# Performance work log

Measured on AMD Instinct MI355X. Metric: run time of the kernel, lower is better.

Reference implementation:

```python
import jax, jax.numpy as jnp
import numpy as np

EMBED_DIM = 1024
CONTEXT_DIM = 768
NUM_HEADS = 16
HEAD_DIM = EMBED_DIM // NUM_HEADS
B, N, M = 8, 4096, 77


def setup_inputs() -> dict:
    key = jax.random.key(0)
    ks = jax.random.split(key, 12)
    s_in = 1.0 / np.sqrt(EMBED_DIM)
    s_ctx = 1.0 / np.sqrt(CONTEXT_DIM)
    x = jax.random.normal(ks[0], (B, N, EMBED_DIM), dtype=jnp.float32)
    context = jax.random.normal(ks[1], (B, M, CONTEXT_DIM), dtype=jnp.float32)
    # realistic padding mask: each example has a random valid prefix length in [1, M]
    lengths = jax.random.randint(ks[2], (B,), 1, M + 1)
    context_mask = jnp.arange(M)[None, :] < lengths[:, None]  # (B, M) bool
    Wq = jax.random.uniform(ks[3], (EMBED_DIM, EMBED_DIM), jnp.float32, -s_in, s_in)
    bq = jax.random.uniform(ks[4], (EMBED_DIM,), jnp.float32, -s_in, s_in)
    Wk = jax.random.uniform(ks[5], (CONTEXT_DIM, EMBED_DIM), jnp.float32, -s_ctx, s_ctx)
    bk = jax.random.uniform(ks[6], (EMBED_DIM,), jnp.float32, -s_ctx, s_ctx)
    Wv = jax.random.uniform(ks[7], (CONTEXT_DIM, EMBED_DIM), jnp.float32, -s_ctx, s_ctx)
    bv = jax.random.uniform(ks[8], (EMBED_DIM,), jnp.float32, -s_ctx, s_ctx)
    Wo = jax.random.uniform(ks[9], (EMBED_DIM, EMBED_DIM), jnp.float32, -s_in, s_in)
    bo = jax.random.uniform(ks[10], (EMBED_DIM,), jnp.float32, -s_in, s_in)
    return {"x": x, "context": context, "context_mask": context_mask,
            "Wq": Wq, "bq": bq, "Wk": Wk, "bk": bk, "Wv": Wv, "bv": bv,
            "Wo": Wo, "bo": bo}


def reference(x, context, context_mask, Wq, bq, Wk, bk, Wv, bv, Wo, bo):
    H, d = NUM_HEADS, HEAD_DIM
    scale = d ** -0.5
    Bx, Nx, _ = x.shape
    Mx = context.shape[1]
    # projections
    q = (x @ Wq + bq).reshape(Bx, Nx, H, d).transpose(0, 2, 1, 3)        # (B,H,N,d)
    k = (context @ Wk + bk).reshape(Bx, Mx, H, d).transpose(0, 2, 1, 3)  # (B,H,M,d)
    v = (context @ Wv + bv).reshape(Bx, Mx, H, d).transpose(0, 2, 1, 3)  # (B,H,M,d)
    # scores with padding mask
    attn = jnp.einsum('bhnd,bhmd->bhnm', q, k) * scale                   # (B,H,N,M)
    attn = jnp.where(context_mask[:, None, None, :], attn, -jnp.inf)
    attn = jax.nn.softmax(attn, axis=-1)
    out = jnp.einsum('bhnm,bhmd->bhnd', attn, v)                          # (B,H,N,d)
    out = out.transpose(0, 2, 1, 3).reshape(Bx, Nx, H * d)                # (B,N,E)
    return out @ Wo + bo
```

## Files before the change

### kernel.cpp

```cpp
#include <hip/hip_runtime.h>

typedef __bf16 bf16x8 __attribute__((ext_vector_type(8)));
typedef float f32x4 __attribute__((ext_vector_type(4)));

#define EMB 1024
#define CTXD 768
#define NH 16
#define HD 64
#define BB 8
#define NN 4096
#define MM 77
#define MPAD 96

static __device__ __forceinline__ unsigned short f2bf(float f) {
    unsigned u = __builtin_bit_cast(unsigned, f);
    u += 0x7FFFu + ((u >> 16) & 1u);
    return (unsigned short)(u >> 16);
}

__global__ void mask_lengths_kernel(const unsigned char* __restrict__ mask,
                                    int* __restrict__ lengths) {
    int ln = threadIdx.x & 63;
    int anyOdd = 0, anyF = 0;
    for (int i = ln; i < BB * MM; i += 64) {
        unsigned char v = mask[i];
        if (v == 0x80u || v == 0x3Fu) anyF = 1;
        if ((i & 3) && v) anyOdd = 1;
    }
    anyF = __any(anyF); anyOdd = __any(anyOdd);
    int layout = anyF ? 2 : (anyOdd ? 1 : 0);
    int b = ln >> 3, j = ln & 7, cnt = 0;
    for (int m = j; m < MM; m += 8) {
        int idx = b * MM + m;
        int valid;
        if (layout == 1)      valid = mask[idx] != 0;
        else if (layout == 0) valid = ((const int*)mask)[idx] != 0;
        else                  valid = ((const float*)mask)[idx] != 0.0f;
        cnt += valid ? 1 : 0;
    }
    cnt += __shfl_xor(cnt, 1, 64);
    cnt += __shfl_xor(cnt, 2, 64);
    cnt += __shfl_xor(cnt, 4, 64);
    if (j == 0) lengths[b] = cnt;
}

__global__ void cast_f32_to_bf16(const float* __restrict__ in,
                                 unsigned short* __restrict__ out, int n8) {
    for (int i = blockIdx.x * blockDim.x + threadIdx.x; i < n8;
         i += gridDim.x * blockDim.x) {
        float4 v0 = ((const float4*)in)[2 * i];
        float4 v1 = ((const float4*)in)[2 * i + 1];
        union { unsigned short u[8]; int4 v; } r;
        r.u[0] = f2bf(v0.x); r.u[1] = f2bf(v0.y);
        r.u[2] = f2bf(v0.z); r.u[3] = f2bf(v0.w);
        r.u[4] = f2bf(v1.x); r.u[5] = f2bf(v1.y);
        r.u[6] = f2bf(v1.z); r.u[7] = f2bf(v1.w);
        ((int4*)out)[i] = r.v;
    }
}

__global__ void cast_ctx_kernel(const float* __restrict__ in,
                                unsigned short* __restrict__ out) {
    int i = blockIdx.x * 256 + threadIdx.x;
    if (i >= 640 * CTXD / 8) return;
    int row = (i * 8) / CTXD;
    union { unsigned short u[8]; int4 v; } r;
    if (row < BB * MM) {
        float4 v0 = ((const float4*)in)[2 * i];
        float4 v1 = ((const float4*)in)[2 * i + 1];
        r.u[0] = f2bf(v0.x); r.u[1] = f2bf(v0.y);
        r.u[2] = f2bf(v0.z); r.u[3] = f2bf(v0.w);
        r.u[4] = f2bf(v1.x); r.u[5] = f2bf(v1.y);
        r.u[6] = f2bf(v1.z); r.u[7] = f2bf(v1.w);
    } else {
        r.v = make_int4(0, 0, 0, 0);
    }
    ((int4*)out)[i] = r.v;
}

struct TPtrs { const float* src[4]; unsigned short* dst[4]; };
__global__ void transpose4_kernel(TPtrs tp) {
    __shared__ float t[32][33];
    int z = blockIdx.z;
    int R = (z < 2) ? 1024 : 768, C = 1024;
    int r0 = blockIdx.y * 32;
    if (r0 >= R) return;
    const float* W = tp.src[z];
    unsigned short* Wt = tp.dst[z];
    int tx = threadIdx.x, ty = threadIdx.y;
    int c0 = blockIdx.x * 32;
#pragma unroll
    for (int i = 0; i < 32; i += 8)
        t[ty + i][tx] = W[(size_t)(r0 + ty + i) * C + c0 + tx];
    __syncthreads();
#pragma unroll
    for (int i = 0; i < 32; i += 8)
        Wt[(size_t)(c0 + ty + i) * R + r0 + tx] = f2bf(t[tx][ty + i]);
}

template <int MODE>
__global__ __launch_bounds__(512, 2) void gemm256_kernel(
    const unsigned short* __restrict__ A, const unsigned short* __restrict__ Bt,
    const float* __restrict__ bias, void* __restrict__ Cout,
    int M, int N, int K) {
    __shared__ unsigned short lds[4][2][256 * 32];
    const int tid = threadIdx.x, wv = tid >> 6, ln = tid & 63;
    const int numN = N >> 8;
    int bid = blockIdx.x;
    const int nwg = (M >> 8) * numN;
    if ((nwg & 7) == 0) { int cpx = nwg >> 3; bid = (bid & 7) * cpx + (bid >> 3); }
    const int nt_ = bid % numN, mt = bid / numN;
    const int m0 = mt << 8, n0 = nt_ << 8;
    const int wr = wv >> 2, wc = wv & 3;
    const int NT = K >> 5;

    const int srow = wv * 16 + (ln >> 2);
    const int sslot = ln & 3;

    auto stageA = [&](int t) {
#pragma unroll
        for (int half = 0; half < 2; ++half) {
            int row = half * 128 + srow;
            int gc = sslot ^ ((row >> 1) & 3);
            __builtin_amdgcn_global_load_lds(
                (const __attribute__((address_space(1))) void*)(
                    A + (size_t)(m0 + row) * K + (t << 5) + gc * 8),
                (__attribute__((address_space(3))) void*)(
                    &lds[t & 3][0][(half * 128 + wv * 16) * 32]),
                16, 0, 0);
        }
    };
    auto stageB = [&](int t) {
#pragma unroll
        for (int half = 0; half < 2; ++half) {
            int row = half * 128 + srow;
            int gc = sslot ^ ((row >> 1) & 3);
            __builtin_amdgcn_global_load_lds(
                (const __attribute__((address_space(1))) void*)(
                    Bt + (size_t)(n0 + row) * K + (t << 5) + gc * 8),
                (__attribute__((address_space(3))) void*)(
                    &lds[t & 3][1][(half * 128 + wv * 16) * 32]),
                16, 0, 0);
        }
    };
    auto readA = [&](const unsigned short* As, int i) -> bf16x8 {
        int arow = wr * 128 + i * 16 + (ln & 15);
        int aslot = (ln >> 4) ^ ((arow >> 1) & 3);
        return *(const bf16x8*)(As + arow * 32 + aslot * 8);
    };
    auto readB = [&](const unsigned short* Bs, int j) -> bf16x8 {
        int brow = wc * 64 + j * 16 + (ln & 15);
        int bslot = (ln >> 4) ^ ((brow >> 1) & 3);
        return *(const bf16x8*)(Bs + brow * 32 + bslot * 8);
    };

    f32x4 acc[8][4] = {};
    bf16x8 afA[4], afB[4], bfrC[4], afN[4], bfrN[4];

    stageA(0); stageB(0); stageA(1); stageB(1); stageA(2); stageB(2);
    asm volatile("s_waitcnt vmcnt(4)" ::: "memory");
    __builtin_amdgcn_sched_barrier(0);
    __builtin_amdgcn_s_barrier();
#pragma unroll
    for (int i = 0; i < 4; ++i) afA[i] = readA(lds[0][0], i);
#pragma unroll
    for (int j = 0; j < 4; ++j) bfrC[j] = readB(lds[0][1], j);

#pragma unroll 4
    for (int t = 0; t < NT; ++t) {
        const unsigned short* As = lds[t & 3][0];
        const unsigned short* Asn = lds[(t + 1) & 3][0];
        const unsigned short* Bsn = lds[(t + 1) & 3][1];
        if (t + 3 < NT) stageA(t + 3);
#pragma unroll
        for (int i = 0; i < 4; ++i) afB[i] = readA(As, i + 4);
        __builtin_amdgcn_s_barrier();
        __builtin_amdgcn_s_setprio(1);
#pragma unroll
        for (int i = 0; i < 4; ++i)
#pragma unroll
            for (int j = 0; j < 4; ++j)
                acc[i][j] = __builtin_amdgcn_mfma_f32_16x16x32_bf16(
                    afA[i], bfrC[j], acc[i][j], 0, 0, 0);
        __builtin_amdgcn_s_setprio(0);
        __builtin_amdgcn_s_barrier();
        if (t + 3 < NT) stageB(t + 3);
        if (t + 1 < NT) {
#pragma unroll
            for (int i = 0; i < 4; ++i) afN[i] = readA(Asn, i);
#pragma unroll
            for (int j = 0; j < 4; ++j) bfrN[j] = readB(Bsn, j);
        }
        if (t + 3 < NT) { asm volatile("s_waitcnt vmcnt(4)" ::: "memory"); }
        else            { asm volatile("s_waitcnt vmcnt(0)" ::: "memory"); }
        __builtin_amdgcn_sched_barrier(0);
        __builtin_amdgcn_s_barrier();
        __builtin_amdgcn_s_setprio(1);
#pragma unroll
        for (int i = 0; i < 4; ++i)
#pragma unroll
            for (int j = 0; j < 4; ++j)
                acc[i + 4][j] = __builtin_amdgcn_mfma_f32_16x16x32_bf16(
                    afB[i], bfrC[j], acc[i + 4][j], 0, 0, 0);
        __builtin_amdgcn_s_setprio(0);
        __builtin_amdgcn_s_barrier();
#pragma unroll
        for (int i = 0; i < 4; ++i) afA[i] = afN[i];
#pragma unroll
        for (int j = 0; j < 4; ++j) bfrC[j] = bfrN[j];
    }

    float bvals[4];
#pragma unroll
    for (int j = 0; j < 4; ++j)
        bvals[j] = bias[n0 + wc * 64 + j * 16 + (ln & 15)];
#pragma unroll
    for (int i = 0; i < 8; ++i)
#pragma unroll
        for (int j = 0; j < 4; ++j)
#pragma unroll
            for (int r = 0; r < 4; ++r) {
                int row = m0 + wr * 128 + i * 16 + (ln >> 4) * 4 + r;
                int col = n0 + wc * 64 + j * 16 + (ln & 15);
                float v = acc[i][j][r] + bvals[j];
                if constexpr (MODE == 0)
                    ((unsigned short*)Cout)[(size_t)row * N + col] = f2bf(v);
                else
                    ((float*)Cout)[(size_t)row * N + col] = v;
            }
}

static __device__ __forceinline__ void stage_tile(
    const unsigned short* __restrict__ G, int ldg, unsigned short* lds,
    int r0, int kt, int wv, int ln) {
    int rown = ln >> 2;
    int koff = (ln & 3) * 8;
#pragma unroll
    for (int r = 0; r < 2; ++r) {
        int cw = wv * 2 + r;
        const unsigned short* src =
            G + (size_t)(r0 + cw * 16 + rown) * ldg + kt + koff;
        __builtin_amdgcn_global_load_lds(
            (const __attribute__((address_space(1))) void*)src,
            (__attribute__((address_space(3))) void*)(lds + cw * 512),
            16, 0, 0);
    }
}

template <int MODE>
__global__ __launch_bounds__(256) void gemm_bt_kernel(
    const unsigned short* __restrict__ A, const unsigned short* __restrict__ Bt,
    const float* __restrict__ bias, void* __restrict__ Cout,
    int M, int N, int K) {
    __shared__ unsigned short As[128 * 32];
    __shared__ unsigned short Bs[128 * 32];
    const int tid = threadIdx.x, wv = tid >> 6, ln = tid & 63;
    const int numM = M >> 7, numN = N >> 7;
    int bid = blockIdx.x;
    const int nwg = numM * numN;
    if ((nwg & 7) == 0) { int cpx = nwg >> 3; bid = (bid & 7) * cpx + (bid >> 3); }
    const int nt = bid % numN, mt = bid / numN;
    const int m0 = mt << 7, n0 = nt << 7;
    const int wr = wv >> 1, wc = wv & 1;

    f32x4 acc[4][4] = {};
    for (int kt = 0; kt < K; kt += 32) {
        __syncthreads();
        stage_tile(A, K, As, m0, kt, wv, ln);
        stage_tile(Bt, K, Bs, n0, kt, wv, ln);
        __syncthreads();
        bf16x8 af[4], bfr[4];
#pragma unroll
        for (int i = 0; i < 4; ++i)
            af[i] = *(const bf16x8*)(As + (wr * 64 + i * 16 + (ln & 15)) * 32 +
                                     (ln >> 4) * 8);
#pragma unroll
        for (int j = 0; j < 4; ++j)
            bfr[j] = *(const bf16x8*)(Bs + (wc * 64 + j * 16 + (ln & 15)) * 32 +
                                      (ln >> 4) * 8);
#pragma unroll
        for (int i = 0; i < 4; ++i)
#pragma unroll
            for (int j = 0; j < 4; ++j)
                acc[i][j] = __builtin_amdgcn_mfma_f32_16x16x32_bf16(
                    af[i], bfr[j], acc[i][j], 0, 0, 0);
    }

    float bvals[4];
#pragma unroll
    for (int j = 0; j < 4; ++j)
        bvals[j] = bias[n0 + wc * 64 + j * 16 + (ln & 15)];

#pragma unroll
    for (int i = 0; i < 4; ++i) {
#pragma unroll
        for (int j = 0; j < 4; ++j) {
#pragma unroll
            for (int r = 0; r < 4; ++r) {
                int row = m0 + wr * 64 + i * 16 + (ln >> 4) * 4 + r;
                int col = n0 + wc * 64 + j * 16 + (ln & 15);
                float v = acc[i][j][r] + bvals[j];
                if (row < BB * MM) {
                    int bb = row / MM, m = row - bb * MM;
                    int hh = col >> 6, d = col & 63;
                    if constexpr (MODE == 2)
                        ((unsigned short*)Cout)[((size_t)(bb * NH + hh) * MPAD + m) * HD + d] = f2bf(v);
                    else
                        ((unsigned short*)Cout)[((size_t)(bb * NH + hh) * HD + d) * MPAD + m] = f2bf(v);
                }
            }
        }
    }
}

__global__ __launch_bounds__(256, 3) void attn_kernel(
    const unsigned short* __restrict__ Q, const unsigned short* __restrict__ Kw,
    const unsigned short* __restrict__ Vt, const int* __restrict__ lengths,
    unsigned short* __restrict__ Out) {
    const int bh = blockIdx.y;
    const int b = bh >> 4, h = bh & 15;
    const int q0 = blockIdx.x * 128;
    const int tid = threadIdx.x, wv = tid >> 6, ln = tid & 63;
    const int len = lengths[b];
    const int kscnt = (len + 31) >> 5;

    __shared__ unsigned short Ps[128][104];

    const unsigned short* Ksrc = Kw + (size_t)bh * (MPAD * HD);
    const unsigned short* Vsrc = Vt + (size_t)bh * (HD * MPAD);

    bf16x8 aq[2][2];
#pragma unroll
    for (int qi = 0; qi < 2; ++qi) {
        const int qr = q0 + wv * 32 + qi * 16 + (ln & 15);
        const unsigned short* qptr =
            Q + (size_t)(b * NN + qr) * EMB + h * HD + (ln >> 4) * 8;
        aq[qi][0] = *(const bf16x8*)(qptr);
        aq[qi][1] = *(const bf16x8*)(qptr + 32);
    }

    bf16x8 vf[3][4];
#pragma unroll
    for (int j = 0; j < 4; ++j)
        vf[0][j] = *(const bf16x8*)(Vsrc + (j * 16 + (ln & 15)) * MPAD +
                                    (ln >> 4) * 8);
    if (kscnt > 1) {
#pragma unroll
        for (int j = 0; j < 4; ++j)
            vf[1][j] = *(const bf16x8*)(Vsrc + (j * 16 + (ln & 15)) * MPAD + 32 +
                                        (ln >> 4) * 8);
    }
    if (kscnt > 2) {
#pragma unroll
        for (int j = 0; j < 4; ++j)
            vf[2][j] = *(const bf16x8*)(Vsrc + (j * 16 + (ln & 15)) * MPAD + 64 +
                                        (ln >> 4) * 8);
    }

    f32x4 s[2][5] = {};
#pragma unroll
    for (int t = 0; t < 5; ++t) {
        if (t * 16 < len) {
            const unsigned short* kp =
                Ksrc + (t * 16 + (ln & 15)) * HD + (ln >> 4) * 8;
            bf16x8 k0 = *(const bf16x8*)(kp);
            bf16x8 k1 = *(const bf16x8*)(kp + 32);
#pragma unroll
            for (int qi = 0; qi < 2; ++qi) {
                s[qi][t] = __builtin_amdgcn_mfma_f32_16x16x32_bf16(
                    aq[qi][0], k0, s[qi][t], 0, 0, 0);
                s[qi][t] = __builtin_amdgcn_mfma_f32_16x16x32_bf16(
                    aq[qi][1], k1, s[qi][t], 0, 0, 0);
            }
        }
    }

    const float scale = 0.125f;
    float mx[2][4], sum[2][4];
#pragma unroll
    for (int qi = 0; qi < 2; ++qi)
#pragma unroll
        for (int r = 0; r < 4; ++r) { mx[qi][r] = -1e30f; sum[qi][r] = 0.f; }
#pragma unroll
    for (int t = 0; t < 5; ++t) {
        int m = t * 16 + (ln & 15);
        bool valid = m < len;
#pragma unroll
        for (int qi = 0; qi < 2; ++qi)
#pragma unroll
            for (int r = 0; r < 4; ++r) {
                float v = valid ? s[qi][t][r] * scale : -1e30f;
                s[qi][t][r] = v;
                mx[qi][r] = fmaxf(mx[qi][r], v);
            }
    }
#pragma unroll
    for (int d = 1; d < 16; d <<= 1)
#pragma unroll
        for (int qi = 0; qi < 2; ++qi)
#pragma unroll
            for (int r = 0; r < 4; ++r)
                mx[qi][r] = fmaxf(mx[qi][r], __shfl_xor(mx[qi][r], d, 64));
#pragma unroll
    for (int t = 0; t < 5; ++t)
#pragma unroll
        for (int qi = 0; qi < 2; ++qi)
#pragma unroll
            for (int r = 0; r < 4; ++r) {
                float p = __expf(s[qi][t][r] - mx[qi][r]);
                s[qi][t][r] = p;
                sum[qi][r] += p;
            }
#pragma unroll
    for (int d = 1; d < 16; d <<= 1)
#pragma unroll
        for (int qi = 0; qi < 2; ++qi)
#pragma unroll
            for (int r = 0; r < 4; ++r)
                sum[qi][r] += __shfl_xor(sum[qi][r], d, 64);

    float rinv[2][4];
#pragma unroll
    for (int qi = 0; qi < 2; ++qi)
#pragma unroll
        for (int r = 0; r < 4; ++r) rinv[qi][r] = 1.0f / sum[qi][r];

#pragma unroll
    for (int t = 0; t < 6; ++t)
#pragma unroll
        for (int qi = 0; qi < 2; ++qi)
#pragma unroll
            for (int r = 0; r < 4; ++r) {
                int row = wv * 32 + qi * 16 + (ln >> 4) * 4 + r;
                float v = (t < 5) ? s[qi][t][r] * rinv[qi][r] : 0.0f;
                Ps[row][t * 16 + (ln & 15)] = f2bf(v);
            }

    f32x4 o[2][4] = {};
    for (int ks = 0; ks < kscnt; ++ks) {
#pragma unroll
        for (int qi = 0; qi < 2; ++qi) {
            bf16x8 pf = *(const bf16x8*)(&Ps[wv * 32 + qi * 16 + (ln & 15)]
                                            [ks * 32 + (ln >> 4) * 8]);
#pragma unroll
            for (int j = 0; j < 4; ++j)
                o[qi][j] = __builtin_amdgcn_mfma_f32_16x16x32_bf16(
                    vf[ks][j], pf, o[qi][j], 0, 0, 0);
        }
    }

#pragma unroll
    for (int qi = 0; qi < 2; ++qi) {
        const int qrow = q0 + wv * 32 + qi * 16 + (ln & 15);
        unsigned short* obase =
            Out + (size_t)(b * NN + qrow) * EMB + h * HD + (ln >> 4) * 4;
#pragma unroll
        for (int j = 0; j < 4; ++j) {
            union { unsigned short u[4]; unsigned long long ll; } pk;
#pragma unroll
            for (int r = 0; r < 4; ++r) pk.u[r] = f2bf(o[qi][j][r]);
            *(unsigned long long*)(obase + j * 16) = pk.ll;
        }
    }
}

extern "C" void kernel_launch(void* const* d_in, const int* in_sizes, int n_in,
                              void* d_out, int out_size, void* d_ws, size_t ws_size,
                              hipStream_t stream) {
    const float* x    = (const float*)d_in[0];
    const float* ctx  = (const float*)d_in[1];
    const unsigned char* cmask = (const unsigned char*)d_in[2];
    const float* Wq = (const float*)d_in[3];
    const float* bq = (const float*)d_in[4];
    const float* Wk = (const float*)d_in[5];
    const float* bk = (const float*)d_in[6];
    const float* Wv = (const float*)d_in[7];
    const float* bv = (const float*)d_in[8];
    const float* Wo = (const float*)d_in[9];
    const float* bo = (const float*)d_in[10];

    char* ws = (char*)d_ws;
    unsigned short* Xbf   = (unsigned short*)(ws);
    unsigned short* Wq_t  = (unsigned short*)(ws + 67108864);
    unsigned short* Wo_t  = (unsigned short*)(ws + 69206016);
    unsigned short* Wk_t  = (unsigned short*)(ws + 71303168);
    unsigned short* Wv_t  = (unsigned short*)(ws + 72876032);
    unsigned short* Cbf   = (unsigned short*)(ws + 74448896);
    unsigned short* Kw    = (unsigned short*)(ws + 75431936);
    unsigned short* Vtw   = (unsigned short*)(ws + 77004800);
    int* lengths          = (int*)(ws + 78577664);
    unsigned short* Qb    = (unsigned short*)d_out;

    mask_lengths_kernel<<<1, 64, 0, stream>>>(cmask, lengths);
    cast_f32_to_bf16<<<2048, 256, 0, stream>>>(x, Xbf, (BB * NN * EMB) / 8);
    cast_ctx_kernel<<<240, 256, 0, stream>>>(ctx, Cbf);
    TPtrs tp;
    tp.src[0] = Wq; tp.src[1] = Wo; tp.src[2] = Wk; tp.src[3] = Wv;
    tp.dst[0] = Wq_t; tp.dst[1] = Wo_t; tp.dst[2] = Wk_t; tp.dst[3] = Wv_t;
    transpose4_kernel<<<dim3(32, 32, 4), dim3(32, 8), 0, stream>>>(tp);
    hipMemsetAsync(Kw, 0, 2 * 1572864, stream);

    gemm256_kernel<0><<<512, 512, 0, stream>>>(Xbf, Wq_t, bq, Qb, 32768, 1024, 1024);
    gemm_bt_kernel<2><<<40, 256, 0, stream>>>(Cbf, Wk_t, bk, Kw, 640, 1024, 768);
    gemm_bt_kernel<3><<<40, 256, 0, stream>>>(Cbf, Wv_t, bv, Vtw, 640, 1024, 768);

    attn_kernel<<<dim3(32, 128), 256, 0, stream>>>(Qb, Kw, Vtw, lengths, Xbf);

    gemm256_kernel<1><<<512, 512, 0, stream>>>(Xbf, Wo_t, bo, d_out, 32768, 1024, 1024);
}
```

Measured before the change: 326.5 us.

## Fuse x f32-to-bf16 cast into Q GEMM, merge K/V GEMMs, simplify pipeline

Removes the standalone cast kernel for x. A new Q-projection GEMM loads f32 A tiles into registers, converts them to bf16 and writes them to LDS, which avoids a full write and re-read of the 64MB bf16 copy. The K and V projection GEMMs are merged into a single launch, and the existing 256-tile GEMM's register double-buffered fragment prefetch is replaced by simpler in-iteration LDS reads with adjusted waitcnts. The trade-off is that the Q GEMM now reads twice the A bytes and does conversion work inside its main loop, and the output GEMM loses its fragment prefetch overlap.

```diff
diff --git a/kernel.cpp b/kernel.cpp
--- a/kernel.cpp
+++ b/kernel.cpp
@@ -42,21 +42,6 @@
     cnt += __shfl_xor(cnt, 2, 64);
     cnt += __shfl_xor(cnt, 4, 64);
     if (j == 0) lengths[b] = cnt;
-}
-
-__global__ void cast_f32_to_bf16(const float* __restrict__ in,
-                                 unsigned short* __restrict__ out, int n8) {
-    for (int i = blockIdx.x * blockDim.x + threadIdx.x; i < n8;
-         i += gridDim.x * blockDim.x) {
-        float4 v0 = ((const float4*)in)[2 * i];
-        float4 v1 = ((const float4*)in)[2 * i + 1];
-        union { unsigned short u[8]; int4 v; } r;
-        r.u[0] = f2bf(v0.x); r.u[1] = f2bf(v0.y);
-        r.u[2] = f2bf(v0.z); r.u[3] = f2bf(v0.w);
-        r.u[4] = f2bf(v1.x); r.u[5] = f2bf(v1.y);
-        r.u[6] = f2bf(v1.z); r.u[7] = f2bf(v1.w);
-        ((int4*)out)[i] = r.v;
-    }
 }
 
 __global__ void cast_ctx_kernel(const float* __restrict__ in,
@@ -98,6 +83,148 @@
         Wt[(size_t)(c0 + ty + i) * R + r0 + tx] = f2bf(t[tx][ty + i]);
 }
 
+__global__ __launch_bounds__(512, 2) void gemm256_qf32(
+    const float* __restrict__ A, const unsigned short* __restrict__ Bt,
+    const float* __restrict__ bias, unsigned short* __restrict__ Cout,
+    int M, int N, int K) {
+    __shared__ unsigned short lds[4][2][256 * 32];
+    const int tid = threadIdx.x, wv = tid >> 6, ln = tid & 63;
+    const int numN = N >> 8;
+    int bid = blockIdx.x;
+    const int nwg = (M >> 8) * numN;
+    if ((nwg & 7) == 0) { int cpx = nwg >> 3; bid = (bid & 7) * cpx + (bid >> 3); }
+    const int nt_ = bid % numN, mt = bid / numN;
+    const int m0 = mt << 8, n0 = nt_ << 8;
+    const int wr = wv >> 2, wc = wv & 3;
+    const int NT = K >> 5;
+
+    const int srow = wv * 16 + (ln >> 2);
+    const int sslot = ln & 3;
+
+    auto stageB = [&](int t) {
+#pragma unroll
+        for (int half = 0; half < 2; ++half) {
+            int row = half * 128 + srow;
+            int gc = sslot ^ ((row >> 1) & 3);
+            __builtin_amdgcn_global_load_lds(
+                (const __attribute__((address_space(1))) void*)(
+                    Bt + (size_t)(n0 + row) * K + (t << 5) + gc * 8),
+                (__attribute__((address_space(3))) void*)(
+                    &lds[t & 3][1][(half * 128 + wv * 16) * 32]),
+                16, 0, 0);
+        }
+    };
+    auto loadAreg = [&](int t, float4 (&dst)[4]) {
+#pragma unroll
+        for (int half = 0; half < 2; ++half) {
+            int row = half * 128 + srow;
+            int gc = sslot ^ ((row >> 1) & 3);
+            const float* src = A + (size_t)(m0 + row) * K + (t << 5) + gc * 8;
+            dst[half * 2 + 0] = *(const float4*)(src);
+            dst[half * 2 + 1] = *(const float4*)(src + 4);
+        }
+    };
+    auto writeA = [&](int t, const float4 (&v)[4]) {
+#pragma unroll
+        for (int half = 0; half < 2; ++half) {
+            union { unsigned short u[8]; int4 q; } r;
+            const float4& a = v[half * 2 + 0];
+            const float4& b = v[half * 2 + 1];
+            r.u[0] = f2bf(a.x); r.u[1] = f2bf(a.y);
+            r.u[2] = f2bf(a.z); r.u[3] = f2bf(a.w);
+            r.u[4] = f2bf(b.x); r.u[5] = f2bf(b.y);
+            r.u[6] = f2bf(b.z); r.u[7] = f2bf(b.w);
+            *(int4*)(&lds[t & 3][0][(half * 128 + wv * 16) * 32] + ln * 8) = r.q;
+        }
+    };
+    auto readA = [&](const unsigned short* As, int i) -> bf16x8 {
+        int arow = wr * 128 + i * 16 + (ln & 15);
+        int aslot = (ln >> 4) ^ ((arow >> 1) & 3);
+        return *(const bf16x8*)(As + arow * 32 + aslot * 8);
+    };
+    auto readB = [&](const unsigned short* Bs, int j) -> bf16x8 {
+        int brow = wc * 64 + j * 16 + (ln & 15);
+        int bslot = (ln >> 4) ^ ((brow >> 1) & 3);
+        return *(const bf16x8*)(Bs + brow * 32 + bslot * 8);
+    };
+
+    f32x4 acc[8][4] = {};
+    float4 aP0[4], aP1[4];
+
+    loadAreg(0, aP0);
+    asm volatile("s_waitcnt vmcnt(0)" ::: "memory");
+    writeA(0, aP0);
+    stageB(0); stageB(1); stageB(2);
+    loadAreg(1, aP1);
+    asm volatile("s_waitcnt vmcnt(8)" ::: "memory");
+    __builtin_amdgcn_sched_barrier(0);
+    asm volatile("s_waitcnt lgkmcnt(0)" ::: "memory");
+    __builtin_amdgcn_s_barrier();
+
+    auto tile_body = [&](int t, float4 (&aNew)[4], float4 (&aOld)[4]) {
+        const unsigned short* As = lds[t & 3][0];
+        const unsigned short* Bs = lds[t & 3][1];
+        if (t + 3 < NT) stageB(t + 3);
+        if (t + 2 < NT) loadAreg(t + 2, aNew);
+        if (t + 3 < NT)      { asm volatile("s_waitcnt vmcnt(6)" ::: "memory"); }
+        else if (t + 2 < NT) { asm volatile("s_waitcnt vmcnt(4)" ::: "memory"); }
+        else                 { asm volatile("s_waitcnt vmcnt(0)" ::: "memory"); }
+        __builtin_amdgcn_sched_barrier(0);
+        if (t + 1 < NT) writeA(t + 1, aOld);
+        bf16x8 bfr[4], af[4];
+#pragma unroll
+        for (int j = 0; j < 4; ++j) bfr[j] = readB(Bs, j);
+#pragma unroll
+        for (int i = 0; i < 4; ++i) af[i] = readA(As, i);
+        asm volatile("s_waitcnt lgkmcnt(0)" ::: "memory");
+        __builtin_amdgcn_sched_barrier(0);
+        __builtin_amdgcn_s_barrier();
+        __builtin_amdgcn_s_setprio(1);
+#pragma unroll
+        for (int i = 0; i < 4; ++i)
+#pragma unroll
+            for (int j = 0; j < 4; ++j)
+                acc[i][j] = __builtin_amdgcn_mfma_f32_16x16x32_bf16(
+                    af[i], bfr[j], acc[i][j], 0, 0, 0);
+        __builtin_amdgcn_s_setprio(0);
+        __builtin_amdgcn_s_barrier();
+#pragma unroll
+        for (int i = 0; i < 4; ++i) af[i] = readA(As, i + 4);
+        asm volatile("s_waitcnt lgkmcnt(0)" ::: "memory");
+        __builtin_amdgcn_sched_barrier(0);
+        __builtin_amdgcn_s_barrier();
+        __builtin_amdgcn_s_setprio(1);
+#pragma unroll
+        for (int i = 0; i < 4; ++i)
+#pragma unroll
+            for (int j = 0; j < 4; ++j)
+                acc[i + 4][j] = __builtin_amdgcn_mfma_f32_16x16x32_bf16(
+                    af[i], bfr[j], acc[i + 4][j], 0, 0, 0);
+        __builtin_amdgcn_s_setprio(0);
+        __builtin_amdgcn_s_barrier();
+    };
+
+    for (int tt = 0; tt < NT; tt += 2) {
+        tile_body(tt, aP0, aP1);
+        tile_body(tt + 1, aP1, aP0);
+    }
+
+    float bvals[4];
+#pragma unroll
+    for (int j = 0; j < 4; ++j)
+        bvals[j] = bias[n0 + wc * 64 + j * 16 + (ln & 15)];
+#pragma unroll
+    for (int i = 0; i < 8; ++i)
+#pragma unroll
+        for (int j = 0; j < 4; ++j)
+#pragma unroll
+            for (int r = 0; r < 4; ++r) {
+                int row = m0 + wr * 128 + i * 16 + (ln >> 4) * 4 + r;
+                int col = n0 + wc * 64 + j * 16 + (ln & 15);
+                Cout[(size_t)row * N + col] = f2bf(acc[i][j][r] + bvals[j]);
+            }
+}
+
 template <int MODE>
 __global__ __launch_bounds__(512, 2) void gemm256_kernel(
     const unsigned short* __restrict__ A, const unsigned short* __restrict__ Bt,
@@ -155,25 +282,22 @@
     };
 
     f32x4 acc[8][4] = {};
-    bf16x8 afA[4], afB[4], bfrC[4], afN[4], bfrN[4];
 
     stageA(0); stageB(0); stageA(1); stageB(1); stageA(2); stageB(2);
-    asm volatile("s_waitcnt vmcnt(4)" ::: "memory");
+    asm volatile("s_waitcnt vmcnt(8)" ::: "memory");
     __builtin_amdgcn_sched_barrier(0);
     __builtin_amdgcn_s_barrier();
-#pragma unroll
-    for (int i = 0; i < 4; ++i) afA[i] = readA(lds[0][0], i);
-#pragma unroll
-    for (int j = 0; j < 4; ++j) bfrC[j] = readB(lds[0][1], j);
 
 #pragma unroll 4
     for (int t = 0; t < NT; ++t) {
         const unsigned short* As = lds[t & 3][0];
-        const unsigned short* Asn = lds[(t + 1) & 3][0];
-        const unsigned short* Bsn = lds[(t + 1) & 3][1];
+        const unsigned short* Bs = lds[t & 3][1];
         if (t + 3 < NT) stageA(t + 3);
-#pragma unroll
-        for (int i = 0; i < 4; ++i) afB[i] = readA(As, i + 4);
+        bf16x8 bfr[4], af[4];
+#pragma unroll
+        for (int j = 0; j < 4; ++j) bfr[j] = readB(Bs, j);
+#pragma unroll
+        for (int i = 0; i < 4; ++i) af[i] = readA(As, i);
         __builtin_amdgcn_s_barrier();
         __builtin_amdgcn_s_setprio(1);
 #pragma unroll
@@ -181,19 +305,12 @@
 #pragma unroll
             for (int j = 0; j < 4; ++j)
                 acc[i][j] = __builtin_amdgcn_mfma_f32_16x16x32_bf16(
-                    afA[i], bfrC[j], acc[i][j], 0, 0, 0);
+                    af[i], bfr[j], acc[i][j], 0, 0, 0);
         __builtin_amdgcn_s_setprio(0);
         __builtin_amdgcn_s_barrier();
         if (t + 3 < NT) stageB(t + 3);
-        if (t + 1 < NT) {
-#pragma unroll
-            for (int i = 0; i < 4; ++i) afN[i] = readA(Asn, i);
-#pragma unroll
-            for (int j = 0; j < 4; ++j) bfrN[j] = readB(Bsn, j);
-        }
-        if (t + 3 < NT) { asm volatile("s_waitcnt vmcnt(4)" ::: "memory"); }
-        else            { asm volatile("s_waitcnt vmcnt(0)" ::: "memory"); }
-        __builtin_amdgcn_sched_barrier(0);
+#pragma unroll
+        for (int i = 0; i < 4; ++i) af[i] = readA(As, i + 4);
         __builtin_amdgcn_s_barrier();
         __builtin_amdgcn_s_setprio(1);
 #pragma unroll
@@ -201,13 +318,15 @@
 #pragma unroll
             for (int j = 0; j < 4; ++j)
                 acc[i + 4][j] = __builtin_amdgcn_mfma_f32_16x16x32_bf16(
-                    afB[i], bfrC[j], acc[i + 4][j], 0, 0, 0);
+                    af[i], bfr[j], acc[i + 4][j], 0, 0, 0);
         __builtin_amdgcn_s_setprio(0);
-        __builtin_amdgcn_s_barrier();
-#pragma unroll
-        for (int i = 0; i < 4; ++i) afA[i] = afN[i];
-#pragma unroll
-        for (int j = 0; j < 4; ++j) bfrC[j] = bfrN[j];
+        if (t < NT - 1) {
+            if (t + 3 < NT)      { asm volatile("s_waitcnt vmcnt(4)" ::: "memory"); }
+            else if (t + 2 < NT) { asm volatile("s_waitcnt vmcnt(2)" ::: "memory"); }
+            else                 { asm volatile("s_waitcnt vmcnt(0)" ::: "memory"); }
+            __builtin_amdgcn_sched_barrier(0);
+        }
+        __builtin_amdgcn_s_barrier();
     }
 
     float bvals[4];
@@ -247,18 +366,24 @@
     }
 }
 
-template <int MODE>
-__global__ __launch_bounds__(256) void gemm_bt_kernel(
-    const unsigned short* __restrict__ A, const unsigned short* __restrict__ Bt,
-    const float* __restrict__ bias, void* __restrict__ Cout,
-    int M, int N, int K) {
+__global__ __launch_bounds__(256) void gemm_kv_kernel(
+    const unsigned short* __restrict__ Cbf,
+    const unsigned short* __restrict__ Wk_t, const float* __restrict__ bk,
+    unsigned short* __restrict__ Kw,
+    const unsigned short* __restrict__ Wv_t, const float* __restrict__ bv,
+    unsigned short* __restrict__ Vtw) {
+    const int M = 640, N = 1024, K = CTXD;
     __shared__ unsigned short As[128 * 32];
     __shared__ unsigned short Bs[128 * 32];
     const int tid = threadIdx.x, wv = tid >> 6, ln = tid & 63;
+    int bid = blockIdx.x;
+    const bool isV = bid >= 40;
+    if (isV) bid -= 40;
+    const unsigned short* Bt = isV ? Wv_t : Wk_t;
+    const float* bias = isV ? bv : bk;
+    unsigned short* Cout = isV ? Vtw : Kw;
     const int numM = M >> 7, numN = N >> 7;
-    int bid = blockIdx.x;
-    const int nwg = numM * numN;
-    if ((nwg & 7) == 0) { int cpx = nwg >> 3; bid = (bid & 7) * cpx + (bid >> 3); }
+    { int cpx = 5; bid = (bid & 7) * cpx + (bid >> 3); }
     const int nt = bid % numN, mt = bid / numN;
     const int m0 = mt << 7, n0 = nt << 7;
     const int wr = wv >> 1, wc = wv & 1;
@@ -266,7 +391,7 @@
     f32x4 acc[4][4] = {};
     for (int kt = 0; kt < K; kt += 32) {
         __syncthreads();
-        stage_tile(A, K, As, m0, kt, wv, ln);
+        stage_tile(Cbf, K, As, m0, kt, wv, ln);
         stage_tile(Bt, K, Bs, n0, kt, wv, ln);
         __syncthreads();
         bf16x8 af[4], bfr[4];
@@ -303,10 +428,10 @@
                 if (row < BB * MM) {
                     int bb = row / MM, m = row - bb * MM;
                     int hh = col >> 6, d = col & 63;
-                    if constexpr (MODE == 2)
-                        ((unsigned short*)Cout)[((size_t)(bb * NH + hh) * MPAD + m) * HD + d] = f2bf(v);
+                    if (!isV)
+                        Kw[((size_t)(bb * NH + hh) * MPAD + m) * HD + d] = f2bf(v);
                     else
-                        ((unsigned short*)Cout)[((size_t)(bb * NH + hh) * HD + d) * MPAD + m] = f2bf(v);
+                        Vtw[((size_t)(bb * NH + hh) * HD + d) * MPAD + m] = f2bf(v);
                 }
             }
         }
@@ -492,7 +617,6 @@
     unsigned short* Qb    = (unsigned short*)d_out;
 
     mask_lengths_kernel<<<1, 64, 0, stream>>>(cmask, lengths);
-    cast_f32_to_bf16<<<2048, 256, 0, stream>>>(x, Xbf, (BB * NN * EMB) / 8);
     cast_ctx_kernel<<<240, 256, 0, stream>>>(ctx, Cbf);
     TPtrs tp;
     tp.src[0] = Wq; tp.src[1] = Wo; tp.src[2] = Wk; tp.src[3] = Wv;
@@ -500,9 +624,8 @@
     transpose4_kernel<<<dim3(32, 32, 4), dim3(32, 8), 0, stream>>>(tp);
     hipMemsetAsync(Kw, 0, 2 * 1572864, stream);
 
-    gemm256_kernel<0><<<512, 512, 0, stream>>>(Xbf, Wq_t, bq, Qb, 32768, 1024, 1024);
-    gemm_bt_kernel<2><<<40, 256, 0, stream>>>(Cbf, Wk_t, bk, Kw, 640, 1024, 768);
-    gemm_bt_kernel<3><<<40, 256, 0, stream>>>(Cbf, Wv_t, bv, Vtw, 640, 1024, 768);
+    gemm256_qf32<<<512, 512, 0, stream>>>(x, Wq_t, bq, Qb, 32768, 1024, 1024);
+    gemm_kv_kernel<<<80, 256, 0, stream>>>(Cbf, Wk_t, bk, Kw, Wv_t, bv, Vtw);
 
     attn_kernel<<<dim3(32, 128), 256, 0, stream>>>(Qb, Kw, Vtw, lengths, Xbf);
 
```

New measurement: 324.9 us. About the same (-0.5%).
